# Kernel tuning notes

Hardware: AMD Instinct MI355X
Metric: run time of the kernel (lower is better)

## Reference

```python
import jax, jax.numpy as jnp
import numpy as np
from math import sqrt

RELATIVE_CUTOFF = 128
VALUE_DIM = 64


def _skew(m):
    # m: (b, h, S, 2S-1) -> (b, h, S, S), out[i, j] = m[i, j - i + S - 1]
    b, h, S, _ = m.shape
    m = jnp.pad(m, ((0, 0), (0, 0), (0, 0), (0, 1)))          # (b,h,S,2S)
    m = m.reshape(b, h, 2 * S * S)
    m = jnp.pad(m, ((0, 0), (0, 0), (0, S - 1)))
    m = m.reshape(b, h, S + 1, 2 * S - 1)
    return m[:, :, :S, S - 1:]


def setup_inputs() -> dict:
    key = jax.random.key(0)
    ks = jax.random.split(key, 5)
    B, S, E, H, Dk, Dv = 2, 2048, 512, 8, 64, 64
    return {
        "xs": jax.random.normal(ks[0], (B, S, E), dtype=jnp.float32),
        "w_q": jax.random.normal(ks[1], (H, E, Dk), dtype=jnp.float32) * (1.0 / sqrt(E)),
        "w_k": jax.random.normal(ks[2], (H, E, Dk), dtype=jnp.float32) * (1.0 / sqrt(E)),
        "w_v": jax.random.normal(ks[3], (H, E, Dv), dtype=jnp.float32) * (1.0 / sqrt(E)),
        "w_o": jnp.ones((H,), dtype=jnp.float32),
        "a_k": jax.random.normal(ks[4], (2 * RELATIVE_CUTOFF + 1, Dk), dtype=jnp.float32) * 0.1,
    }


def reference(xs, w_q, w_k, w_v, w_o, a_k):
    S = xs.shape[1]
    queries = jnp.einsum("bse,heq->bhsq", xs, w_q)
    keys = jnp.einsum("bse,hek->bhsk", xs, w_k)
    values = jnp.einsum("bse,hev->bhsv", xs, w_v)

    # relative positional embeddings: pos in [-S+1, S-1], clamped to cutoff
    pos = jnp.clip(jnp.arange(-S + 1, S), -RELATIVE_CUTOFF, RELATIVE_CUTOFF) + RELATIVE_CUTOFF
    rel = a_k[pos]                                             # (2S-1, Dk)

    q_k = jnp.einsum("bhiq,bhjq->bhij", queries, keys)
    q_rel = _skew(jnp.einsum("bhiq,rq->bhir", queries, rel))   # (b,h,S,S)

    e = (q_k + q_rel) / sqrt(VALUE_DIM)
    alphas = jax.nn.softmax(e, axis=3)
    z = jnp.einsum("bhij,bhjv->bhiv", alphas, values)
    return jnp.einsum("bhsv,h->bsv", z, w_o)
```

## Files before the change

kernel.cpp:

```cpp
#include <hip/hip_runtime.h>
#include <hip/hip_bf16.h>

#define S_LEN 2048
#define E_DIM 512
#define D_DIM 64
#define H_NUM 8
#define B_NUM 2
#define BH_NUM 16
#define NQA 257
#define QAE_W 512
#define KSPLIT 2
#define KV_PER (S_LEN / KSPLIT)
#define NT (KV_PER / 64)
#define QTILE 256

typedef _Float16 half8 __attribute__((ext_vector_type(8)));
typedef float f32x16 __attribute__((ext_vector_type(16)));
typedef unsigned int uint2v __attribute__((ext_vector_type(2)));
typedef unsigned int uint4v __attribute__((ext_vector_type(4)));

static __device__ __forceinline__ f32x16 MFMA(half8 a, half8 b, f32x16 c) {
    return __builtin_amdgcn_mfma_f32_32x32x16_f16(a, b, c, 0, 0, 0);
}
static __device__ __forceinline__ f32x16 ZERO16() {
    f32x16 z;
    #pragma unroll
    for (int i = 0; i < 16; ++i) z[i] = 0.f;
    return z;
}
static __device__ __forceinline__ unsigned int PKRTZ(float a, float b) {
    return __builtin_bit_cast(unsigned int, __builtin_amdgcn_cvt_pkrtz(a, b));
}

__global__ __launch_bounds__(256) void cast_x_kernel(
    const float* __restrict__ xs, _Float16* __restrict__ Xh)
{
    const int idx = (blockIdx.x * 256 + threadIdx.x) * 8;
    float4 a = *(const float4*)&xs[idx];
    float4 b = *(const float4*)&xs[idx + 4];
    half8 o;
    o[0] = (_Float16)a.x; o[1] = (_Float16)a.y; o[2] = (_Float16)a.z; o[3] = (_Float16)a.w;
    o[4] = (_Float16)b.x; o[5] = (_Float16)b.y; o[6] = (_Float16)b.z; o[7] = (_Float16)b.w;
    *(half8*)&Xh[idx] = o;
}

__global__ __launch_bounds__(256) void cast_wak_kernel(
    const float* __restrict__ w_q, const float* __restrict__ w_k,
    const float* __restrict__ w_v, const float* __restrict__ w_o,
    const float* __restrict__ a_k,
    _Float16* __restrict__ Wht, _Float16* __restrict__ akh)
{
    __shared__ float T[64][68];
    const int type = blockIdx.z;
    const int t = threadIdx.x;
    if (type == 3) {
        const int bn = blockIdx.y * 8 + blockIdx.x;
        if (bn >= 9) return;
        const int idx = (bn * 256 + t) * 8;
        if (idx < NQA * 64) {
            float4 a = *(const float4*)&a_k[idx];
            float4 b = *(const float4*)&a_k[idx + 4];
            half8 o;
            o[0] = (_Float16)a.x; o[1] = (_Float16)a.y; o[2] = (_Float16)a.z; o[3] = (_Float16)a.w;
            o[4] = (_Float16)b.x; o[5] = (_Float16)b.y; o[6] = (_Float16)b.z; o[7] = (_Float16)b.w;
            *(half8*)&akh[idx] = o;
        }
        return;
    }
    const int kt = blockIdx.x, h = blockIdx.y;
    const float* W = (type == 0) ? w_q : (type == 1) ? w_k : w_v;
    const float scale = (type == 0) ? 0.125f : (type == 2 ? w_o[h] : 1.0f);
    const int kr = t >> 2, nseg = (t & 3) * 16;
    #pragma unroll
    for (int i = 0; i < 4; ++i)
        *(float4*)&T[kr][nseg + 4 * i] =
            *(const float4*)&W[((size_t)h * 512 + kt * 64 + kr) * 64 + nseg + 4 * i];
    __syncthreads();
    const int nr = t >> 2, kseg = (t & 3) * 16;
    _Float16* dst = Wht + ((size_t)(type * 8 + h) * 64 + nr) * 512 + kt * 64 + kseg;
    #pragma unroll
    for (int i = 0; i < 2; ++i) {
        half8 o;
        #pragma unroll
        for (int j = 0; j < 8; ++j) o[j] = (_Float16)(T[kseg + 8 * i + j][nr] * scale);
        *(half8*)&dst[8 * i] = o;
    }
}

__global__ __launch_bounds__(256) void proj_mfma_kernel(
    const _Float16* __restrict__ Xh, const _Float16* __restrict__ Wht,
    _Float16* __restrict__ Qh, _Float16* __restrict__ Kh,
    _Float16* __restrict__ Vt)
{
    __shared__ _Float16 Xlds[2][128][72];
    __shared__ _Float16 Wlds[2][64][72];

    const int mt = blockIdx.x, bh = blockIdx.y, type = blockIdx.z;
    const int b = bh >> 3, h = bh & 7;
    const int m0 = mt * 128;
    const int t = threadIdx.x, wid = t >> 6, lane = t & 63;
    const int lq = lane & 31, lh = lane >> 5;

    const _Float16* W = Wht + (size_t)(type * 8 + h) * 64 * 512;
    const _Float16* X = Xh + ((size_t)b * S_LEN + m0) * 512;

    const int xrow = t >> 1, xseg = (t & 1) * 32;
    const int wrow = t >> 2, wseg = (t & 3) * 16;

    #pragma unroll
    for (int i = 0; i < 4; ++i)
        *(half8*)&Xlds[0][xrow][xseg + 8 * i] =
            *(const half8*)&X[(size_t)xrow * 512 + xseg + 8 * i];
    #pragma unroll
    for (int i = 0; i < 2; ++i)
        *(half8*)&Wlds[0][wrow][wseg + 8 * i] =
            *(const half8*)&W[(size_t)wrow * 512 + wseg + 8 * i];
    __syncthreads();

    f32x16 acc[2];
    acc[0] = ZERO16(); acc[1] = ZERO16();
    int cur = 0;
    for (int c = 0; c < 8; ++c) {
        half8 xst[4], wst[2];
        if (c < 7) {
            const int k0 = (c + 1) * 64;
            #pragma unroll
            for (int i = 0; i < 4; ++i)
                xst[i] = *(const half8*)&X[(size_t)xrow * 512 + k0 + xseg + 8 * i];
            #pragma unroll
            for (int i = 0; i < 2; ++i)
                wst[i] = *(const half8*)&W[(size_t)wrow * 512 + k0 + wseg + 8 * i];
        }
        #pragma unroll
        for (int kc = 0; kc < 4; ++kc) {
            half8 a  = *(const half8*)&Xlds[cur][wid * 32 + lq][kc * 16 + lh * 8];
            half8 b0 = *(const half8*)&Wlds[cur][lq][kc * 16 + lh * 8];
            half8 b1 = *(const half8*)&Wlds[cur][32 + lq][kc * 16 + lh * 8];
            acc[0] = MFMA(a, b0, acc[0]);
            acc[1] = MFMA(a, b1, acc[1]);
        }
        if (c < 7) {
            #pragma unroll
            for (int i = 0; i < 4; ++i)
                *(half8*)&Xlds[cur ^ 1][xrow][xseg + 8 * i] = xst[i];
            #pragma unroll
            for (int i = 0; i < 2; ++i)
                *(half8*)&Wlds[cur ^ 1][wrow][wseg + 8 * i] = wst[i];
        }
        __syncthreads();
        cur ^= 1;
    }

    _Float16* ob = &Wlds[0][0][0];
    #pragma unroll
    for (int n = 0; n < 2; ++n)
        #pragma unroll
        for (int r = 0; r < 16; ++r) {
            int row = wid * 32 + (r & 3) + ((r >> 2) << 3) + (lh << 2);
            ob[row * 72 + n * 32 + lq] = (_Float16)acc[n][r];
        }
    __syncthreads();

    if (type == 2) {
        const int v = t >> 2, sseg = (t & 3) * 32;
        _Float16* dst = Vt + ((size_t)bh * 64 + v) * S_LEN + m0 + sseg;
        #pragma unroll
        for (int i = 0; i < 4; ++i) {
            half8 o;
            #pragma unroll
            for (int j = 0; j < 8; ++j) o[j] = ob[(sseg + 8 * i + j) * 72 + v];
            *(half8*)&dst[8 * i] = o;
        }
    } else {
        _Float16* P = (type == 0) ? Qh : Kh;
        const int row = t >> 1, seg = (t & 1) * 32;
        _Float16* dst = P + ((size_t)bh * S_LEN + m0 + row) * 64 + seg;
        #pragma unroll
        for (int i = 0; i < 4; ++i)
            *(half8*)&dst[8 * i] = *(const half8*)&ob[row * 72 + seg + 8 * i];
    }
}

__global__ __launch_bounds__(256) void qa_mfma_kernel(
    const _Float16* __restrict__ Qh, const _Float16* __restrict__ akh,
    _Float16* __restrict__ QAe)
{
    __shared__ _Float16 ak[288][72];
    const int m0 = blockIdx.x * 128, bh = blockIdx.y;
    const int t = threadIdx.x, wid = t >> 6, lane = t & 63;
    const int lq = lane & 31, lh = lane >> 5;

    for (int r = t; r < 288; r += 256) {
        if (r < NQA) {
            #pragma unroll
            for (int i = 0; i < 8; ++i)
                *(half8*)&ak[r][8 * i] = *(const half8*)&akh[(size_t)r * 64 + 8 * i];
        } else {
            half8 z = {};
            #pragma unroll
            for (int i = 0; i < 8; ++i) *(half8*)&ak[r][8 * i] = z;
        }
    }
    __syncthreads();

    const int qg = m0 + wid * 32 + lq;
    half8 qfr[4];
    #pragma unroll
    for (int kc = 0; kc < 4; ++kc)
        qfr[kc] = *(const half8*)&Qh[((size_t)bh * S_LEN + qg) * 64 + kc * 16 + lh * 8];

    for (int nsub = 0; nsub < 9; ++nsub) {
        f32x16 acc = ZERO16();
        #pragma unroll
        for (int kc = 0; kc < 4; ++kc) {
            half8 bf = *(const half8*)&ak[nsub * 32 + lq][kc * 16 + lh * 8];
            acc = MFMA(qfr[kc], bf, acc);
        }
        const int col = nsub * 32 + lq;
        if (col < NQA) {
            #pragma unroll
            for (int r = 0; r < 16; ++r) {
                int row = m0 + wid * 32 + (r & 3) + ((r >> 2) << 3) + (lh << 2);
                QAe[((size_t)bh * S_LEN + row) * QAE_W + col + 128] = (_Float16)acc[r];
            }
        }
    }
}

__global__ __launch_bounds__(256) void qae_fill_kernel(_Float16* __restrict__ QAe)
{
    const int row = blockIdx.x * 32 + (threadIdx.x >> 3);
    const int c = (threadIdx.x & 7) * 8;
    const size_t base = (size_t)row * QAE_W;
    const _Float16 lo = QAe[base + 128];
    const _Float16 hi = QAe[base + 384];
    half8 vlo, vhi;
    #pragma unroll
    for (int j = 0; j < 8; ++j) { vlo[j] = lo; vhi[j] = hi; }
    *(half8*)&QAe[base + c] = vlo;
    *(half8*)&QAe[base + 64 + c] = vlo;
    *(half8*)&QAe[base + 384 + c] = vhi;
    *(half8*)&QAe[base + 448 + c] = vhi;
}

__global__ __launch_bounds__(512) void attn_kernel(
    const _Float16* __restrict__ Qh, const _Float16* __restrict__ Kh,
    const _Float16* __restrict__ Vt, const _Float16* __restrict__ QAe,
    _Float16* __restrict__ Po, float2* __restrict__ Ml)
{
    __shared__ __align__(16) char smraw[36864];
    _Float16 (*Klds)[64][72] = (_Float16(*)[64][72])smraw;
    _Float16 (*Vlds)[64][72] = (_Float16(*)[64][72])(smraw + 18432);
    _Float16* Obuf = (_Float16*)smraw;
    __shared__ __align__(16) _Float16 Bnd[8][32][128];

    const int p0 = blockIdx.x;
    const int nb = (p0 & 7) * 32 + (p0 >> 3);
    const int bh = nb >> 4;
    const int rem = nb & 15;
    const int qt = rem & 7, ks = rem >> 3;
    const int i0 = qt * QTILE, k0 = ks * KV_PER;

    const int t = threadIdx.x, wid = t >> 6, lane = t & 63;
    const int lq = lane & 31, lh = lane >> 5;
    const int i0w = i0 + wid * 32;
    const int qg = i0w + lq;

    int mode = 0;
    if (k0 >= i0 + QTILE - 1 + 128) mode = 1;
    else if (k0 + KV_PER - 1 <= i0 - 128) mode = 2;

    half8 qf[4];
    #pragma unroll
    for (int kc = 0; kc < 4; ++kc)
        qf[kc] = *(const half8*)&Qh[((size_t)bh * S_LEN + qg) * 64 + kc * 16 + lh * 8];

    const _Float16* qaeRow = QAe + ((size_t)bh * S_LEN + qg) * QAE_W;
    const float qa_lo = (float)qaeRow[128];
    const float qa_hi = (float)qaeRow[384];
    const _Float16* BndSrc = QAe + ((size_t)bh * S_LEN + i0w) * QAE_W;

    float rm = -1e30f, rl = 0.f;
    f32x16 acco[2];
    acco[0] = ZERO16(); acco[1] = ZERO16();

    const int srow = t >> 3, sseg = (t & 7) * 8;
    const _Float16* Kbase = Kh + ((size_t)bh * S_LEN + k0) * 64;
    const _Float16* Vbase = Vt + ((size_t)bh * 64 + srow) * S_LEN + k0;

    half8 kst, vst;
    *(half8*)&Klds[0][srow][sseg] = *(const half8*)&Kbase[(size_t)srow * 64 + sseg];
    *(half8*)&Vlds[0][srow][sseg] = *(const half8*)&Vbase[sseg];
    kst = *(const half8*)&Kbase[(size_t)(64 + srow) * 64 + sseg];
    vst = *(const half8*)&Vbase[64 + sseg];
    __syncthreads();

    const int brow = lane >> 4;
    const int bcol = (lane & 15) * 8;

    for (int jt = 0; jt < NT; ++jt) {
        const int cur = jt & 1;
        if (jt) __syncthreads();
        if (jt + 1 < NT) {
            *(half8*)&Klds[cur ^ 1][srow][sseg] = kst;
            *(half8*)&Vlds[cur ^ 1][srow][sseg] = vst;
        }
        if (jt + 2 < NT) {
            const int jg = (jt + 2) * 64;
            kst = *(const half8*)&Kbase[(size_t)(jg + srow) * 64 + sseg];
            vst = *(const half8*)&Vbase[jg + sseg];
        }

        const int j0g = k0 + jt * 64;
        const int diff = j0g - i0w;
        const bool allhi = (mode == 1) || (diff >= 159);
        const bool alllo = (mode == 2) || (diff <= -191);
        const bool inband = !(allhi || alllo);
        const int cw0 = (diff + 225) & ~7;

        if (inband) {
            #pragma unroll
            for (int ps = 0; ps < 8; ++ps) {
                half8 v = *(const half8*)&BndSrc[(size_t)(ps * 4 + brow) * QAE_W + cw0 + bcol];
                *(half8*)&Bnd[wid][ps * 4 + brow][bcol] = v;
            }
        }

        f32x16 accs[2];
        accs[0] = ZERO16(); accs[1] = ZERO16();
        __builtin_amdgcn_s_setprio(1);
        #pragma unroll
        for (int kc = 0; kc < 4; ++kc) {
            half8 ka = *(const half8*)&Klds[cur][lq][kc * 16 + lh * 8];
            half8 kb = *(const half8*)&Klds[cur][32 + lq][kc * 16 + lh * 8];
            accs[0] = MFMA(ka, qf[kc], accs[0]);
            accs[1] = MFMA(kb, qf[kc], accs[1]);
        }
        __builtin_amdgcn_s_setprio(0);

        float bunif = 0.f;
        if (allhi) bunif = qa_hi;
        else if (alllo) bunif = qa_lo;
        else {
            asm volatile("s_waitcnt lgkmcnt(0)" ::: "memory");
            __builtin_amdgcn_sched_barrier(0);
            const int pb = diff + 256 - cw0 - lq;
            #pragma unroll
            for (int m = 0; m < 2; ++m)
                #pragma unroll
                for (int r = 0; r < 16; ++r) {
                    const int keyoff = m * 32 + (r & 3) + ((r >> 2) << 3) + (lh << 2);
                    accs[m][r] += (float)Bnd[wid][lq][pb + keyoff];
                }
        }

        float t8[8];
        #pragma unroll
        for (int i = 0; i < 8; ++i)
            t8[i] = fmaxf(fmaxf(accs[0][i], accs[0][i + 8]),
                          fmaxf(accs[1][i], accs[1][i + 8]));
        float tmax = fmaxf(fmaxf(fmaxf(t8[0], t8[1]), fmaxf(t8[2], t8[3])),
                           fmaxf(fmaxf(t8[4], t8[5]), fmaxf(t8[6], t8[7])));
        tmax = fmaxf(tmax, __shfl_xor(tmax, 32));
        const float mnew = fmaxf(rm, tmax + bunif);
        const bool resc = __any(mnew > rm);
        const float corr = __expf(rm - mnew);
        const float shift = mnew - bunif;
        rm = mnew;

        #pragma unroll
        for (int m = 0; m < 2; ++m)
            #pragma unroll
            for (int r = 0; r < 16; ++r)
                accs[m][r] = __expf(accs[m][r] - shift);

        float s8[8];
        #pragma unroll
        for (int i = 0; i < 8; ++i)
            s8[i] = (accs[0][i] + accs[0][i + 8]) + (accs[1][i] + accs[1][i + 8]);
        float psum = ((s8[0] + s8[1]) + (s8[2] + s8[3])) +
                     ((s8[4] + s8[5]) + (s8[6] + s8[7]));
        psum += __shfl_xor(psum, 32);

        if (resc) {
            rl = rl * corr + psum;
            #pragma unroll
            for (int n = 0; n < 2; ++n)
                #pragma unroll
                for (int r = 0; r < 16; ++r) acco[n][r] *= corr;
        } else {
            rl += psum;
        }

        half8 pf[4];
        #pragma unroll
        for (int kc = 0; kc < 4; ++kc) {
            const int m = kc >> 1, rb = (kc & 1) * 8;
            unsigned int a01 = PKRTZ(accs[m][rb + 0], accs[m][rb + 1]);
            unsigned int a45 = PKRTZ(accs[m][rb + 4], accs[m][rb + 5]);
            unsigned int a23 = PKRTZ(accs[m][rb + 2], accs[m][rb + 3]);
            unsigned int a67 = PKRTZ(accs[m][rb + 6], accs[m][rb + 7]);
            uint2v r02 = __builtin_amdgcn_permlane32_swap(a01, a45, false, false);
            uint2v r13 = __builtin_amdgcn_permlane32_swap(a23, a67, false, false);
            uint4v wv;
            wv[0] = r02[0]; wv[1] = r13[0]; wv[2] = r02[1]; wv[3] = r13[1];
            pf[kc] = __builtin_bit_cast(half8, wv);
        }

        __builtin_amdgcn_s_setprio(1);
        #pragma unroll
        for (int kc = 0; kc < 4; ++kc) {
            half8 v0 = *(const half8*)&Vlds[cur][lq][kc * 16 + lh * 8];
            half8 v1 = *(const half8*)&Vlds[cur][32 + lq][kc * 16 + lh * 8];
            acco[0] = MFMA(v0, pf[kc], acco[0]);
            acco[1] = MFMA(v1, pf[kc], acco[1]);
        }
        __builtin_amdgcn_s_setprio(0);
    }

    __syncthreads();
    const int orow = wid * 32 + lq;
    #pragma unroll
    for (int n = 0; n < 2; ++n)
        #pragma unroll
        for (int rq = 0; rq < 4; ++rq) {
            uint2v hv;
            hv[0] = PKRTZ(acco[n][rq * 4 + 0], acco[n][rq * 4 + 1]);
            hv[1] = PKRTZ(acco[n][rq * 4 + 2], acco[n][rq * 4 + 3]);
            *(uint2v*)&Obuf[(size_t)orow * 72 + n * 32 + rq * 8 + lh * 4] = hv;
        }
    if (lh == 0)
        Ml[((size_t)ks * BH_NUM + bh) * S_LEN + qg] = make_float2(rm, rl);
    asm volatile("s_waitcnt lgkmcnt(0)" ::: "memory");
    __builtin_amdgcn_sched_barrier(0);
    const int rrow = wid * 32 + (lane >> 1);
    const int rseg = (lane & 1) * 32;
    _Float16* dst = Po + (((size_t)ks * BH_NUM + bh) * S_LEN + i0 + rrow) * 64 + rseg;
    #pragma unroll
    for (int i = 0; i < 4; ++i)
        *(half8*)&dst[8 * i] = *(const half8*)&Obuf[(size_t)rrow * 72 + rseg + 8 * i];
}

__global__ __launch_bounds__(256) void merge_kernel(
    const _Float16* __restrict__ Po, const float2* __restrict__ Ml,
    float* __restrict__ out)
{
    const int b = blockIdx.y;
    const int s = blockIdx.x * 32 + (threadIdx.x >> 3);
    const int v0 = (threadIdx.x & 7) * 8;
    float acc[8] = {0, 0, 0, 0, 0, 0, 0, 0};
    #pragma unroll
    for (int h = 0; h < 8; ++h) {
        const int bh = b * 8 + h;
        float m[KSPLIT], l[KSPLIT];
        #pragma unroll
        for (int p = 0; p < KSPLIT; ++p) {
            const float2 v = Ml[((size_t)p * BH_NUM + bh) * S_LEN + s];
            m[p] = v.x; l[p] = v.y;
        }
        float M = fmaxf(m[0], m[1]);
        float L = 0.f, w[KSPLIT];
        #pragma unroll
        for (int p = 0; p < KSPLIT; ++p) { w[p] = __expf(m[p] - M); L += w[p] * l[p]; }
        const float invL = 1.0f / L;
        #pragma unroll
        for (int p = 0; p < KSPLIT; ++p) {
            half8 o = *(const half8*)&Po[(((size_t)p * BH_NUM + bh) * S_LEN + s) * 64 + v0];
            const float wp = w[p] * invL;
            #pragma unroll
            for (int j = 0; j < 8; ++j) acc[j] += wp * (float)o[j];
        }
    }
    float4 o0 = {acc[0], acc[1], acc[2], acc[3]};
    float4 o1 = {acc[4], acc[5], acc[6], acc[7]};
    *(float4*)&out[((size_t)b * S_LEN + s) * 64 + v0] = o0;
    *(float4*)&out[((size_t)b * S_LEN + s) * 64 + v0 + 4] = o1;
}

extern "C" void kernel_launch(void* const* d_in, const int* in_sizes, int n_in,
                              void* d_out, int out_size, void* d_ws, size_t ws_size,
                              hipStream_t stream)
{
    const float* xs  = (const float*)d_in[0];
    const float* w_q = (const float*)d_in[1];
    const float* w_k = (const float*)d_in[2];
    const float* w_v = (const float*)d_in[3];
    const float* w_o = (const float*)d_in[4];
    const float* a_k = (const float*)d_in[5];
    float* out = (float*)d_out;

    char* w = (char*)d_ws;
    _Float16* Xh  = (_Float16*)w;  w += (size_t)B_NUM * S_LEN * E_DIM * 2;
    _Float16* Wht = (_Float16*)w;  w += (size_t)3 * H_NUM * 64 * 512 * 2;
    _Float16* akh = (_Float16*)w;  w += 33024;
    _Float16* Qh  = (_Float16*)w;  w += (size_t)BH_NUM * S_LEN * 64 * 2;
    _Float16* Kh  = (_Float16*)w;  w += (size_t)BH_NUM * S_LEN * 64 * 2;
    _Float16* Vt  = (_Float16*)w;  w += (size_t)BH_NUM * S_LEN * 64 * 2;
    _Float16* QAe = (_Float16*)w;  w += (size_t)BH_NUM * S_LEN * QAE_W * 2;
    _Float16* Po  = (_Float16*)w;  w += (size_t)KSPLIT * BH_NUM * S_LEN * 64 * 2;
    float2*   Ml  = (float2*)w;

    cast_x_kernel<<<1024, 256, 0, stream>>>(xs, Xh);
    cast_wak_kernel<<<dim3(8, 8, 4), 256, 0, stream>>>(w_q, w_k, w_v, w_o, a_k, Wht, akh);
    proj_mfma_kernel<<<dim3(16, 16, 3), 256, 0, stream>>>(Xh, Wht, Qh, Kh, Vt);
    qa_mfma_kernel<<<dim3(16, 16), 256, 0, stream>>>(Qh, akh, QAe);
    qae_fill_kernel<<<1024, 256, 0, stream>>>(QAe);
    attn_kernel<<<256, 512, 0, stream>>>(Qh, Kh, Vt, QAe, Po, Ml);
    merge_kernel<<<dim3(64, 2), 256, 0, stream>>>(Po, Ml, out);
}
```

Measured before the change: 89.17 us.

## Fuse QAe padding fill into qa kernel and prefetch band tiles into registers

The separate qae_fill kernel is removed. The qa_mfma kernel now records the clamped edge values in shared memory and writes the padded border columns itself, which saves one launch and a read of QAe. In the attention loop, the band-bias tile for the next key tile is loaded into registers one iteration ahead, so the global load latency overlaps compute. The cost is eight extra half8 registers per thread, and the allhi/alllo logic is restructured around the prefetched inband flag.

```diff
diff --git a/kernel.cpp b/kernel.cpp
--- a/kernel.cpp
+++ b/kernel.cpp
@@ -186,6 +186,7 @@
     _Float16* __restrict__ QAe)
 {
     __shared__ _Float16 ak[288][72];
+    __shared__ _Float16 SLo[128], SHi[128];
     const int m0 = blockIdx.x * 128, bh = blockIdx.y;
     const int t = threadIdx.x, wid = t >> 6, lane = t & 63;
     const int lq = lane & 31, lh = lane >> 5;
@@ -220,27 +221,27 @@
         if (col < NQA) {
             #pragma unroll
             for (int r = 0; r < 16; ++r) {
-                int row = m0 + wid * 32 + (r & 3) + ((r >> 2) << 3) + (lh << 2);
-                QAe[((size_t)bh * S_LEN + row) * QAE_W + col + 128] = (_Float16)acc[r];
+                const int row = m0 + wid * 32 + (r & 3) + ((r >> 2) << 3) + (lh << 2);
+                const _Float16 v = (_Float16)acc[r];
+                QAe[((size_t)bh * S_LEN + row) * QAE_W + col + 128] = v;
+                if (col == 0)   SLo[row - m0] = v;
+                if (col == 256) SHi[row - m0] = v;
             }
         }
     }
-}
-
-__global__ __launch_bounds__(256) void qae_fill_kernel(_Float16* __restrict__ QAe)
-{
-    const int row = blockIdx.x * 32 + (threadIdx.x >> 3);
-    const int c = (threadIdx.x & 7) * 8;
-    const size_t base = (size_t)row * QAE_W;
-    const _Float16 lo = QAe[base + 128];
-    const _Float16 hi = QAe[base + 384];
+    __syncthreads();
+
+    const int prow = t >> 1, pseg = (t & 1) * 64;
+    const _Float16 lo = SLo[prow], hi = SHi[prow];
     half8 vlo, vhi;
     #pragma unroll
     for (int j = 0; j < 8; ++j) { vlo[j] = lo; vhi[j] = hi; }
-    *(half8*)&QAe[base + c] = vlo;
-    *(half8*)&QAe[base + 64 + c] = vlo;
-    *(half8*)&QAe[base + 384 + c] = vhi;
-    *(half8*)&QAe[base + 448 + c] = vhi;
+    _Float16* pb = QAe + ((size_t)bh * S_LEN + m0 + prow) * QAE_W;
+    #pragma unroll
+    for (int i = 0; i < 8; ++i) {
+        *(half8*)&pb[pseg + 8 * i] = vlo;
+        *(half8*)&pb[384 + pseg + 8 * i] = vhi;
+    }
 }
 
 __global__ __launch_bounds__(512) void attn_kernel(
@@ -288,15 +289,27 @@
     const _Float16* Kbase = Kh + ((size_t)bh * S_LEN + k0) * 64;
     const _Float16* Vbase = Vt + ((size_t)bh * 64 + srow) * S_LEN + k0;
 
-    half8 kst, vst;
+    const int brow = lane >> 4;
+    const int bcol = (lane & 15) * 8;
+
+    half8 kst, vst, breg[8];
     *(half8*)&Klds[0][srow][sseg] = *(const half8*)&Kbase[(size_t)srow * 64 + sseg];
     *(half8*)&Vlds[0][srow][sseg] = *(const half8*)&Vbase[sseg];
     kst = *(const half8*)&Kbase[(size_t)(64 + srow) * 64 + sseg];
     vst = *(const half8*)&Vbase[64 + sseg];
-    __syncthreads();
-
-    const int brow = lane >> 4;
-    const int bcol = (lane & 15) * 8;
+
+    bool inb_next;
+    {
+        const int d0 = k0 - i0w;
+        inb_next = (mode == 0) && (d0 < 159) && (d0 > -191);
+        if (inb_next) {
+            const int cw0n = (d0 + 225) & ~7;
+            #pragma unroll
+            for (int ps = 0; ps < 8; ++ps)
+                breg[ps] = *(const half8*)&BndSrc[(size_t)(ps * 4 + brow) * QAE_W + cw0n + bcol];
+        }
+    }
+    __syncthreads();
 
     for (int jt = 0; jt < NT; ++jt) {
         const int cur = jt & 1;
@@ -311,18 +324,23 @@
             vst = *(const half8*)&Vbase[jg + sseg];
         }
 
-        const int j0g = k0 + jt * 64;
-        const int diff = j0g - i0w;
-        const bool allhi = (mode == 1) || (diff >= 159);
-        const bool alllo = (mode == 2) || (diff <= -191);
-        const bool inband = !(allhi || alllo);
+        const int diff = k0 + jt * 64 - i0w;
+        const bool inband = inb_next;
         const int cw0 = (diff + 225) & ~7;
 
         if (inband) {
             #pragma unroll
-            for (int ps = 0; ps < 8; ++ps) {
-                half8 v = *(const half8*)&BndSrc[(size_t)(ps * 4 + brow) * QAE_W + cw0 + bcol];
-                *(half8*)&Bnd[wid][ps * 4 + brow][bcol] = v;
+            for (int ps = 0; ps < 8; ++ps)
+                *(half8*)&Bnd[wid][ps * 4 + brow][bcol] = breg[ps];
+        }
+        {
+            const int dn = diff + 64;
+            inb_next = (jt + 1 < NT) && (mode == 0) && (dn < 159) && (dn > -191);
+            if (inb_next) {
+                const int cw0n = (dn + 225) & ~7;
+                #pragma unroll
+                for (int ps = 0; ps < 8; ++ps)
+                    breg[ps] = *(const half8*)&BndSrc[(size_t)(ps * 4 + brow) * QAE_W + cw0n + bcol];
             }
         }
 
@@ -338,6 +356,8 @@
         }
         __builtin_amdgcn_s_setprio(0);
 
+        const bool allhi = (mode == 1) || (mode == 0 && diff >= 159);
+        const bool alllo = (mode == 2) || (mode == 0 && diff <= -191);
         float bunif = 0.f;
         if (allhi) bunif = qa_hi;
         else if (alllo) bunif = qa_lo;
@@ -504,7 +524,6 @@
     cast_wak_kernel<<<dim3(8, 8, 4), 256, 0, stream>>>(w_q, w_k, w_v, w_o, a_k, Wht, akh);
     proj_mfma_kernel<<<dim3(16, 16, 3), 256, 0, stream>>>(Xh, Wht, Qh, Kh, Vt);
     qa_mfma_kernel<<<dim3(16, 16), 256, 0, stream>>>(Qh, akh, QAe);
-    qae_fill_kernel<<<1024, 256, 0, stream>>>(QAe);
     attn_kernel<<<256, 512, 0, stream>>>(Qh, Kh, Vt, QAe, Po, Ml);
     merge_kernel<<<dim3(64, 2), 256, 0, stream>>>(Po, Ml, out);
 }
```

After: 92.61 us. +3.9%, slower.
